# Performance work log

Hardware: AMD Instinct MI355X
Metric: run time of the kernel (lower is better)

Reference implementation:

```python
import jax, jax.numpy as jnp
import numpy as np

LATENT_DIM = 128
NUM_QUANTIZERS = 8
CODEBOOK_SIZE = 1024


def setup_inputs() -> dict:
    key = jax.random.key(0)
    k1, k2 = jax.random.split(key)
    z = jax.random.normal(k1, (8, LATENT_DIM, 4096), dtype=jnp.float32)
    scale = 1.0 / np.sqrt(LATENT_DIM)
    codebooks = jax.random.uniform(
        k2, (NUM_QUANTIZERS, CODEBOOK_SIZE, LATENT_DIM),
        minval=-scale, maxval=scale, dtype=jnp.float32)
    return {"z": z, "codebooks": codebooks}


def _nearest_indices(x_flat, codebook):
    # x_flat: [N, D], codebook: [K, D] -> [N] argmin of squared L2 distance
    d = (jnp.sum(x_flat * x_flat, axis=1, keepdims=True)
         - 2.0 * x_flat @ codebook.T
         + jnp.sum(codebook * codebook, axis=1)[None, :])
    return jnp.argmin(d, axis=1)


def reference(z, codebooks):
    # z: [B, D, S] -> z_bsd: [B, S, D]
    z_bsd = jnp.transpose(z, (0, 2, 1))
    B, S, D = z_bsd.shape
    Q, K, _ = codebooks.shape

    residual = z_bsd
    quantized = jnp.zeros_like(z_bsd)
    idx_list = []
    for q in range(Q):  # small fixed loop over quantizer stages
        cb = codebooks[q]
        idx = _nearest_indices(residual.reshape(-1, D), cb).reshape(B, S)
        selected = cb[idx]                       # [B, S, D] gather
        quantized = quantized + selected
        residual = residual - jax.lax.stop_gradient(selected)
        idx_list.append(idx)
    indices = jnp.stack(idx_list, axis=-1)        # [B, S, Q]

    commitment_loss = jnp.mean(
        (z_bsd - jax.lax.stop_gradient(quantized)) ** 2)
    quantized_st = z_bsd + jax.lax.stop_gradient(quantized - z_bsd)

    def _perplexity(ix):  # ix: [B, S] codes for one quantizer
        counts = jnp.zeros((K,), jnp.float32).at[ix.reshape(-1)].add(1.0)
        probs = counts / jnp.maximum(counts.sum(), 1.0)
        entropy = -jnp.sum(probs * jnp.log(probs + 1e-10))
        return jnp.exp(entropy)

    perplexity = jnp.mean(jax.vmap(_perplexity, in_axes=2)(indices))

    return (jnp.transpose(quantized_st, (0, 2, 1)),  # [B, D, S]
            indices, commitment_loss, perplexity)
```

## Files before the change

kernel.cpp:

```cpp
#include <hip/hip_runtime.h>
#include <math.h>
#include <stdint.h>

#define D       128
#define KCODES  1024
#define NQ      8
#define BATCH   8
#define SLEN    4096
#define NPTS    (BATCH*SLEN)
#define TM      64

typedef __attribute__((address_space(1))) const void GV;
typedef __attribute__((address_space(3))) void LV;
__device__ __forceinline__ void gload16(const void* g, void* l) {
    __builtin_amdgcn_global_load_lds((GV*)g, (LV*)l, 16, 0, 0);
}

__global__ void k_zero(int* hist, double* csum) {
    int t = blockIdx.x * blockDim.x + threadIdx.x;
    if (t < NQ * KCODES) hist[t] = 0;
    if (t == 0) *csum = 0.0;
}

__global__ void k_c2(const float* __restrict__ cbs, float* __restrict__ c2f) {
    int i = blockIdx.x * blockDim.x + threadIdx.x;
    const float* row = cbs + (size_t)i * D;
    float r8[8];
    #pragma unroll
    for (int j = 0; j < 8; ++j) r8[j] = __fmul_rn(row[j], row[j]);
    for (int d = 8; d < 128; d += 8)
        #pragma unroll
        for (int j = 0; j < 8; ++j)
            r8[j] = __fadd_rn(r8[j], __fmul_rn(row[d + j], row[d + j]));
    float s01 = __fadd_rn(r8[0], r8[1]);
    float s23 = __fadd_rn(r8[2], r8[3]);
    float s45 = __fadd_rn(r8[4], r8[5]);
    float s67 = __fadd_rn(r8[6], r8[7]);
    c2f[i] = __fadd_rn(__fadd_rn(s01, s23), __fadd_rn(s45, s67));
}

__global__ __launch_bounds__(256) void k_init(const float* __restrict__ z,
                                              float* __restrict__ resid,
                                              float* __restrict__ quant) {
    __shared__ float xt[64][129];
    int b = blockIdx.x >> 6, st = blockIdx.x & 63;
    int s0 = st * 64;
    for (int it = 0; it < 32; ++it) {
        int flat = it * 256 + threadIdx.x;
        int d = flat >> 6, sl = flat & 63;
        xt[sl][d] = z[((size_t)(b * D + d)) * SLEN + s0 + sl];
    }
    __syncthreads();
    for (int it = 0; it < 8; ++it) {
        int flat = it * 256 + threadIdx.x;
        int sl = flat >> 5, dq = (flat & 31) * 4;
        size_t o = (size_t)(b * SLEN + s0 + sl) * D + dq;
        float4 r;
        r.x = xt[sl][dq]; r.y = xt[sl][dq + 1];
        r.z = xt[sl][dq + 2]; r.w = xt[sl][dq + 3];
        *(float4*)(resid + o) = r;
        float4 zz; zz.x = zz.y = zz.z = zz.w = 0.0f;
        *(float4*)(quant + o) = zz;
    }
}

__global__ __launch_bounds__(256, 2) void k_argmin(const float* __restrict__ cb,
                                                   const float* __restrict__ c2,
                                                   const float* __restrict__ resid,
                                                   float* __restrict__ pbest,
                                                   int* __restrict__ pidx) {
    __shared__ __align__(16) float xs[TM][132];
    __shared__ __align__(16) float cs[4][2][512];
    __shared__ __align__(16) float ccl[4][128];
    __shared__ float redS[4][TM];
    __shared__ int   redI[4][TM];

    int tid = threadIdx.x;
    int u = blockIdx.x;
    int pblk = u >> 1, half = u & 1;
    int pbase = pblk * TM;
    int l = tid & 63, w = tid >> 6;
    int pl = l & 7, cl = l >> 3;

    const char* cwb = (const char*)cb + ((size_t)(half * 512 + w * 128) << 9);
    char* csw = (char*)&cs[w][0][0];
    const char* xsb = (const char*)&xs[0][0];

    int lanoff = ((l >> 1) << 9) + ((l & 1) << 4);

#define ISSUE(T) { \
    const char* _src = cwb + (((T) >> 4) << 15) + (((T) & 15) << 5) + lanoff; \
    char* _dst = csw + (((T) & 1) << 11); \
    gload16(_src,             _dst); \
    gload16(_src + (1 << 14), _dst + 1024); }

    ISSUE(0);
    if (l < 32) {
        float4 cv = *(const float4*)(c2 + half * 512 + w * 128 + l * 4);
        *(float4*)&ccl[w][l * 4] = cv;
    }

    #pragma unroll
    for (int it = 0; it < 8; ++it) {
        int e = (it * 256 + tid) * 4;
        int p = e >> 7, d = e & 127;
        *(float4*)&xs[p][d] = *(const float4*)(resid + (size_t)(pbase + p) * D + d);
    }
    __syncthreads();

    if (tid < TM) {
        float r8[8];
        #pragma unroll
        for (int j = 0; j < 8; ++j) r8[j] = __fmul_rn(xs[tid][j], xs[tid][j]);
        for (int i = 8; i < 128; i += 8)
            #pragma unroll
            for (int j = 0; j < 8; ++j)
                r8[j] = __fadd_rn(r8[j], __fmul_rn(xs[tid][i + j], xs[tid][i + j]));
        float s01 = __fadd_rn(r8[0], r8[1]);
        float s23 = __fadd_rn(r8[2], r8[3]);
        float s45 = __fadd_rn(r8[4], r8[5]);
        float s67 = __fadd_rn(r8[6], r8[7]);
        xs[tid][128] = __fadd_rn(__fadd_rn(s01, s23), __fadd_rn(s45, s67));
    }
    __syncthreads();

    float acc[8][8];
    #pragma unroll
    for (int i = 0; i < 8; ++i)
        #pragma unroll
        for (int j = 0; j < 8; ++j) acc[i][j] = 0.0f;
    float best[8]; int bidx[8];
    #pragma unroll
    for (int i = 0; i < 8; ++i) { best[i] = 3.4e38f; bidx[i] = 0; }

    #pragma unroll 1
    for (int t = 0; t < 32; ++t) {
        if (t < 31) {
            ISSUE(t + 1);
            asm volatile("s_waitcnt vmcnt(2)" ::: "memory");
        } else {
            asm volatile("s_waitcnt vmcnt(0)" ::: "memory");
        }
        const char* cbuf = csw + ((t & 1) << 11) + (cl << 5);
        const char* xrow = xsb + pl * 528 + ((t & 15) << 5);
        float4 cfa[8], cfb[8];
        #pragma unroll
        for (int j = 0; j < 8; ++j) {
            cfa[j] = *(const float4*)(cbuf + (j << 8));
            cfb[j] = *(const float4*)(cbuf + (j << 8) + 16);
        }
        #pragma unroll
        for (int i = 0; i < 8; ++i) {
            float4 xA = *(const float4*)(xrow + i * 4224);
            float4 xB = *(const float4*)(xrow + i * 4224 + 16);
            #pragma unroll
            for (int j = 0; j < 8; ++j) {
                float a = acc[i][j];
                a = __fmaf_rn(xA.x, cfa[j].x, a);
                a = __fmaf_rn(xA.y, cfa[j].y, a);
                a = __fmaf_rn(xA.z, cfa[j].z, a);
                a = __fmaf_rn(xA.w, cfa[j].w, a);
                a = __fmaf_rn(xB.x, cfb[j].x, a);
                a = __fmaf_rn(xB.y, cfb[j].y, a);
                a = __fmaf_rn(xB.z, cfb[j].z, a);
                a = __fmaf_rn(xB.w, cfb[j].w, a);
                acc[i][j] = a;
            }
        }
        if ((t & 15) == 15) {
            int c = t >> 4;
            #pragma unroll
            for (int i = 0; i < 8; ++i) {
                float xxv = xs[pl + 8 * i][128];
                #pragma unroll
                for (int j = 0; j < 8; ++j) {
                    float cc = ccl[w][(c << 6) + cl + (j << 3)];
                    int k = half * 512 + (w << 7) + (c << 6) + cl + (j << 3);
                    float t1  = __fadd_rn(xxv, __fmul_rn(-2.0f, acc[i][j]));
                    float dsc = __fadd_rn(t1, cc);
                    if (dsc < best[i]) { best[i] = dsc; bidx[i] = k; }
                    acc[i][j] = 0.0f;
                }
            }
        }
    }

    #pragma unroll
    for (int i = 0; i < 8; ++i) {
        float b = best[i]; int bi = bidx[i];
        #pragma unroll
        for (int off = 8; off < 64; off <<= 1) {
            float b2 = __shfl_xor(b, off, 64);
            int  bi2 = __shfl_xor(bi, off, 64);
            if (b2 < b || (b2 == b && bi2 < bi)) { b = b2; bi = bi2; }
        }
        if (cl == 0) { redS[w][pl + 8 * i] = b; redI[w][pl + 8 * i] = bi; }
    }
    __syncthreads();
    if (tid < TM) {
        float b = redS[0][tid]; int bi = redI[0][tid];
        #pragma unroll
        for (int ww = 1; ww < 4; ++ww) {
            float b2 = redS[ww][tid]; int bi2 = redI[ww][tid];
            if (b2 < b || (b2 == b && bi2 < bi)) { b = b2; bi = bi2; }
        }
        pbest[half * NPTS + pbase + tid] = b;
        pidx [half * NPTS + pbase + tid] = bi;
    }
#undef ISSUE
}

__global__ void k_update(const float* __restrict__ cb,
                         const float* __restrict__ pbest,
                         const int* __restrict__ pidx,
                         int* __restrict__ idx,
                         float* __restrict__ resid, float* __restrict__ quant) {
    int gid = blockIdx.x * blockDim.x + threadIdx.x;
    int n = gid >> 5, d4 = (gid & 31) * 4;
    float a = pbest[n], b = pbest[NPTS + n];
    int ia = pidx[n], ib = pidx[NPTS + n];
    int k = (b < a) ? ib : ia;
    if ((gid & 31) == 0) idx[n] = k;
    float4 c = *(const float4*)(cb + (size_t)k * D + d4);
    size_t o = (size_t)n * D + d4;
    float4 r = *(const float4*)(resid + o);
    float4 q = *(const float4*)(quant + o);
    r.x = __fsub_rn(r.x, c.x); r.y = __fsub_rn(r.y, c.y);
    r.z = __fsub_rn(r.z, c.z); r.w = __fsub_rn(r.w, c.w);
    q.x = __fadd_rn(q.x, c.x); q.y = __fadd_rn(q.y, c.y);
    q.z = __fadd_rn(q.z, c.z); q.w = __fadd_rn(q.w, c.w);
    *(float4*)(resid + o) = r;
    *(float4*)(quant + o) = q;
}

__global__ __launch_bounds__(256) void k_out0(const float* __restrict__ z,
                                              const float* __restrict__ quant,
                                              float* __restrict__ out0,
                                              double* __restrict__ csum) {
    __shared__ float xt[64][129];
    __shared__ double wsum[4];
    int b = blockIdx.x >> 6, st = blockIdx.x & 63;
    int s0 = st * 64;
    for (int it = 0; it < 8; ++it) {
        int flat = it * 256 + threadIdx.x;
        int sl = flat >> 5, dq = (flat & 31) * 4;
        float4 q = *(const float4*)(quant + (size_t)(b * SLEN + s0 + sl) * D + dq);
        xt[sl][dq] = q.x; xt[sl][dq + 1] = q.y;
        xt[sl][dq + 2] = q.z; xt[sl][dq + 3] = q.w;
    }
    __syncthreads();
    double v = 0.0;
    for (int it = 0; it < 32; ++it) {
        int flat = it * 256 + threadIdx.x;
        int d = flat >> 6, sl = flat & 63;
        size_t o = ((size_t)(b * D + d)) * SLEN + s0 + sl;
        float zz = z[o], qq = xt[sl][d];
        out0[o] = __fadd_rn(zz, __fsub_rn(qq, zz));
        float e = __fsub_rn(zz, qq);
        v += (double)e * (double)e;
    }
    for (int off = 32; off > 0; off >>= 1) v += __shfl_down(v, off, 64);
    int lane = threadIdx.x & 63, wv = threadIdx.x >> 6;
    if (lane == 0) wsum[wv] = v;
    __syncthreads();
    if (threadIdx.x == 0) {
        double tsum = wsum[0] + wsum[1] + wsum[2] + wsum[3];
        atomicAdd(csum, tsum);
    }
}

__global__ void k_outidx(const int* __restrict__ idx, float* __restrict__ out1) {
    int o = blockIdx.x * blockDim.x + threadIdx.x;
    int q = o & 7, n = o >> 3;
    out1[o] = (float)idx[q * NPTS + n];
}

__global__ void k_hist(const int* __restrict__ idx, int* __restrict__ hist) {
    int o = blockIdx.x * blockDim.x + threadIdx.x;
    int q = o >> 15;
    atomicAdd(&hist[q * KCODES + idx[o]], 1);
}

__global__ __launch_bounds__(256) void k_final(const int* __restrict__ hist,
                                               const double* __restrict__ csum,
                                               float* __restrict__ outs) {
    __shared__ double sh[256];
    double perp = 0.0;
    for (int q = 0; q < NQ; ++q) {
        double h = 0.0;
        for (int k = threadIdx.x; k < KCODES; k += 256) {
            double p = (double)hist[q * KCODES + k] / (double)NPTS;
            h -= p * log(p + 1e-10);
        }
        sh[threadIdx.x] = h; __syncthreads();
        for (int off = 128; off > 0; off >>= 1) {
            if (threadIdx.x < off) sh[threadIdx.x] += sh[threadIdx.x + off];
            __syncthreads();
        }
        if (threadIdx.x == 0) perp += exp(sh[0]);
        __syncthreads();
    }
    if (threadIdx.x == 0) {
        outs[0] = (float)(*csum / (double)((size_t)NPTS * D));
        outs[1] = (float)(perp / (double)NQ);
    }
}

extern "C" void kernel_launch(void* const* d_in, const int* in_sizes, int n_in,
                              void* d_out, int out_size, void* d_ws, size_t ws_size,
                              hipStream_t stream) {
    const float* z  = (const float*)d_in[0];
    const float* cb = (const float*)d_in[1];
    float* out0 = (float*)d_out;
    float* out1 = out0 + 4194304;
    float* outs = out1 + 262144;

    char* w = (char*)d_ws;
    float* resid  = (float*)w;
    float* quant  = (float*)(w + 16777216);
    int*   idx    = (int*)(w + 33554432);
    int*   hist   = (int*)(w + 34603008);
    double* csum  = (double*)(w + 34635776);
    float* c2f    = (float*)(w + 34635840);
    float* pbest  = (float*)(w + 34668608);
    int*   pidx   = (int*)(w + 34930752);

    k_zero<<<32, 256, 0, stream>>>(hist, csum);
    k_c2<<<32, 256, 0, stream>>>(cb, c2f);
    k_init<<<512, 256, 0, stream>>>(z, resid, quant);

    for (int q = 0; q < NQ; ++q) {
        const float* cbq = cb + (size_t)q * KCODES * D;
        k_argmin<<<2 * NPTS / TM, 256, 0, stream>>>(cbq, c2f + q * KCODES, resid,
                                                    pbest, pidx);
        k_update<<<NPTS * 32 / 256, 256, 0, stream>>>(cbq, pbest, pidx,
                                                      idx + q * NPTS, resid, quant);
    }

    k_out0<<<512, 256, 0, stream>>>(z, quant, out0, csum);
    k_outidx<<<NPTS * NQ / 256, 256, 0, stream>>>(idx, out1);
    k_hist<<<NPTS * NQ / 256, 256, 0, stream>>>(idx, hist);
    k_final<<<1, 256, 0, stream>>>(hist, csum, outs);
}
```

Measured before the change: 1.080 ms.

## Transpose residual tile in LDS and use packed FP32 FMA for distance dot products

```diff
diff --git a/kernel.cpp b/kernel.cpp
--- a/kernel.cpp
+++ b/kernel.cpp
@@ -10,11 +10,20 @@
 #define NPTS    (BATCH*SLEN)
 #define TM      64
 
+typedef __attribute__((ext_vector_type(2))) float f32x2;
+
 typedef __attribute__((address_space(1))) const void GV;
 typedef __attribute__((address_space(3))) void LV;
 __device__ __forceinline__ void gload16(const void* g, void* l) {
     __builtin_amdgcn_global_load_lds((GV*)g, (LV*)l, 16, 0, 0);
 }
+
+#define PKFMA_LO(A, X, CP) \
+    asm("v_pk_fma_f32 %0, %1, %2, %0 op_sel_hi:[1,0,1]" \
+        : "+v"(A) : "v"(X), "v"(CP))
+#define PKFMA_HI(A, X, CP) \
+    asm("v_pk_fma_f32 %0, %1, %2, %0 op_sel:[0,1,0] op_sel_hi:[1,1,1]" \
+        : "+v"(A) : "v"(X), "v"(CP))
 
 __global__ void k_zero(int* hist, double* csum) {
     int t = blockIdx.x * blockDim.x + threadIdx.x;
@@ -69,7 +78,7 @@
                                                    const float* __restrict__ resid,
                                                    float* __restrict__ pbest,
                                                    int* __restrict__ pidx) {
-    __shared__ __align__(16) float xs[TM][132];
+    __shared__ __align__(16) float xst[129][64];
     __shared__ __align__(16) float cs[4][2][512];
     __shared__ __align__(16) float ccl[4][128];
     __shared__ float redS[4][TM];
@@ -84,7 +93,7 @@
 
     const char* cwb = (const char*)cb + ((size_t)(half * 512 + w * 128) << 9);
     char* csw = (char*)&cs[w][0][0];
-    const char* xsb = (const char*)&xs[0][0];
+    float* xstf = &xst[0][0];
 
     int lanoff = ((l >> 1) << 9) + ((l & 1) << 4);
 
@@ -102,33 +111,41 @@
 
     #pragma unroll
     for (int it = 0; it < 8; ++it) {
-        int e = (it * 256 + tid) * 4;
-        int p = e >> 7, d = e & 127;
-        *(float4*)&xs[p][d] = *(const float4*)(resid + (size_t)(pbase + p) * D + d);
-    }
-    __syncthreads();
-
+        int g = it * 4 + w;
+        float4 v = *(const float4*)(resid + (size_t)(pbase + l) * D + 4 * g);
+        xstf[(size_t)(4 * g + 0) * 64 + l] = v.x;
+        xstf[(size_t)(4 * g + 1) * 64 + l] = v.y;
+        xstf[(size_t)(4 * g + 2) * 64 + l] = v.z;
+        xstf[(size_t)(4 * g + 3) * 64 + l] = v.w;
+    }
     if (tid < TM) {
+        const float* row = resid + (size_t)(pbase + tid) * D;
         float r8[8];
         #pragma unroll
-        for (int j = 0; j < 8; ++j) r8[j] = __fmul_rn(xs[tid][j], xs[tid][j]);
-        for (int i = 8; i < 128; i += 8)
-            #pragma unroll
-            for (int j = 0; j < 8; ++j)
-                r8[j] = __fadd_rn(r8[j], __fmul_rn(xs[tid][i + j], xs[tid][i + j]));
+        for (int j = 0; j < 8; ++j) r8[j] = 0.0f;
+        #pragma unroll
+        for (int g = 0; g < 32; ++g) {
+            float4 v = *(const float4*)(row + 4 * g);
+            int b = (g & 1) * 4;
+            r8[b + 0] = __fadd_rn(r8[b + 0], __fmul_rn(v.x, v.x));
+            r8[b + 1] = __fadd_rn(r8[b + 1], __fmul_rn(v.y, v.y));
+            r8[b + 2] = __fadd_rn(r8[b + 2], __fmul_rn(v.z, v.z));
+            r8[b + 3] = __fadd_rn(r8[b + 3], __fmul_rn(v.w, v.w));
+        }
         float s01 = __fadd_rn(r8[0], r8[1]);
         float s23 = __fadd_rn(r8[2], r8[3]);
         float s45 = __fadd_rn(r8[4], r8[5]);
         float s67 = __fadd_rn(r8[6], r8[7]);
-        xs[tid][128] = __fadd_rn(__fadd_rn(s01, s23), __fadd_rn(s45, s67));
-    }
-    __syncthreads();
-
-    float acc[8][8];
-    #pragma unroll
-    for (int i = 0; i < 8; ++i)
-        #pragma unroll
-        for (int j = 0; j < 8; ++j) acc[i][j] = 0.0f;
+        xstf[(size_t)128 * 64 + tid] = __fadd_rn(__fadd_rn(s01, s23),
+                                                 __fadd_rn(s45, s67));
+    }
+    __syncthreads();
+
+    f32x2 accp[4][8];
+    #pragma unroll
+    for (int m = 0; m < 4; ++m)
+        #pragma unroll
+        for (int j = 0; j < 8; ++j) { accp[m][j].x = 0.0f; accp[m][j].y = 0.0f; }
     float best[8]; int bidx[8];
     #pragma unroll
     for (int i = 0; i < 8; ++i) { best[i] = 3.4e38f; bidx[i] = 0; }
@@ -142,59 +159,80 @@
             asm volatile("s_waitcnt vmcnt(0)" ::: "memory");
         }
         const char* cbuf = csw + ((t & 1) << 11) + (cl << 5);
-        const char* xrow = xsb + pl * 528 + ((t & 15) << 5);
-        float4 cfa[8], cfb[8];
+        const float* xrow = xstf + (size_t)((t & 15) << 3) * 64 + (pl << 3);
+        f32x2 xA[8], xB[8], xC[8], xD[8];
+        #pragma unroll
+        for (int d = 0; d < 8; ++d) {
+            float4 q = *(const float4*)(xrow + (size_t)d * 64);
+            float4 r = *(const float4*)(xrow + (size_t)d * 64 + 4);
+            const f32x2* qp = (const f32x2*)&q;
+            const f32x2* rp = (const f32x2*)&r;
+            xA[d] = qp[0]; xB[d] = qp[1]; xC[d] = rp[0]; xD[d] = rp[1];
+        }
         #pragma unroll
         for (int j = 0; j < 8; ++j) {
-            cfa[j] = *(const float4*)(cbuf + (j << 8));
-            cfb[j] = *(const float4*)(cbuf + (j << 8) + 16);
-        }
-        #pragma unroll
-        for (int i = 0; i < 8; ++i) {
-            float4 xA = *(const float4*)(xrow + i * 4224);
-            float4 xB = *(const float4*)(xrow + i * 4224 + 16);
+            float4 cfa = *(const float4*)(cbuf + (j << 8));
+            float4 cfb = *(const float4*)(cbuf + (j << 8) + 16);
+            const f32x2* ca = (const f32x2*)&cfa;
+            const f32x2* cb2 = (const f32x2*)&cfb;
+            f32x2 a0 = accp[0][j], a1 = accp[1][j];
+            f32x2 a2 = accp[2][j], a3 = accp[3][j];
+            PKFMA_LO(a0, xA[0], ca[0]);  PKFMA_LO(a1, xB[0], ca[0]);
+            PKFMA_LO(a2, xC[0], ca[0]);  PKFMA_LO(a3, xD[0], ca[0]);
+            PKFMA_HI(a0, xA[1], ca[0]);  PKFMA_HI(a1, xB[1], ca[0]);
+            PKFMA_HI(a2, xC[1], ca[0]);  PKFMA_HI(a3, xD[1], ca[0]);
+            PKFMA_LO(a0, xA[2], ca[1]);  PKFMA_LO(a1, xB[2], ca[1]);
+            PKFMA_LO(a2, xC[2], ca[1]);  PKFMA_LO(a3, xD[2], ca[1]);
+            PKFMA_HI(a0, xA[3], ca[1]);  PKFMA_HI(a1, xB[3], ca[1]);
+            PKFMA_HI(a2, xC[3], ca[1]);  PKFMA_HI(a3, xD[3], ca[1]);
+            PKFMA_LO(a0, xA[4], cb2[0]); PKFMA_LO(a1, xB[4], cb2[0]);
+            PKFMA_LO(a2, xC[4], cb2[0]); PKFMA_LO(a3, xD[4], cb2[0]);
+            PKFMA_HI(a0, xA[5], cb2[0]); PKFMA_HI(a1, xB[5], cb2[0]);
+            PKFMA_HI(a2, xC[5], cb2[0]); PKFMA_HI(a3, xD[5], cb2[0]);
+            PKFMA_LO(a0, xA[6], cb2[1]); PKFMA_LO(a1, xB[6], cb2[1]);
+            PKFMA_LO(a2, xC[6], cb2[1]); PKFMA_LO(a3, xD[6], cb2[1]);
+            PKFMA_HI(a0, xA[7], cb2[1]); PKFMA_HI(a1, xB[7], cb2[1]);
+            PKFMA_HI(a2, xC[7], cb2[1]); PKFMA_HI(a3, xD[7], cb2[1]);
+            accp[0][j] = a0; accp[1][j] = a1;
+            accp[2][j] = a2; accp[3][j] = a3;
+        }
+        if ((t & 15) == 15) {
+            int c = t >> 4;
+            float xxv[8];
+            #pragma unroll
+            for (int lp = 0; lp < 8; ++lp)
+                xxv[lp] = xstf[(size_t)128 * 64 + 8 * pl + lp];
             #pragma unroll
             for (int j = 0; j < 8; ++j) {
-                float a = acc[i][j];
-                a = __fmaf_rn(xA.x, cfa[j].x, a);
-                a = __fmaf_rn(xA.y, cfa[j].y, a);
-                a = __fmaf_rn(xA.z, cfa[j].z, a);
-                a = __fmaf_rn(xA.w, cfa[j].w, a);
-                a = __fmaf_rn(xB.x, cfb[j].x, a);
-                a = __fmaf_rn(xB.y, cfb[j].y, a);
-                a = __fmaf_rn(xB.z, cfb[j].z, a);
-                a = __fmaf_rn(xB.w, cfb[j].w, a);
-                acc[i][j] = a;
-            }
-        }
-        if ((t & 15) == 15) {
-            int c = t >> 4;
-            #pragma unroll
-            for (int i = 0; i < 8; ++i) {
-                float xxv = xs[pl + 8 * i][128];
+                float cc = ccl[w][(c << 6) + cl + (j << 3)];
+                int k = half * 512 + (w << 7) + (c << 6) + cl + (j << 3);
                 #pragma unroll
-                for (int j = 0; j < 8; ++j) {
-                    float cc = ccl[w][(c << 6) + cl + (j << 3)];
-                    int k = half * 512 + (w << 7) + (c << 6) + cl + (j << 3);
-                    float t1  = __fadd_rn(xxv, __fmul_rn(-2.0f, acc[i][j]));
-                    float dsc = __fadd_rn(t1, cc);
-                    if (dsc < best[i]) { best[i] = dsc; bidx[i] = k; }
-                    acc[i][j] = 0.0f;
+                for (int m = 0; m < 4; ++m) {
+                    f32x2 av = accp[m][j];
+                    float t1, dsc;
+                    t1  = __fadd_rn(xxv[2 * m], __fmul_rn(-2.0f, av.x));
+                    dsc = __fadd_rn(t1, cc);
+                    if (dsc < best[2 * m])     { best[2 * m] = dsc;     bidx[2 * m] = k; }
+                    t1  = __fadd_rn(xxv[2 * m + 1], __fmul_rn(-2.0f, av.y));
+                    dsc = __fadd_rn(t1, cc);
+                    if (dsc < best[2 * m + 1]) { best[2 * m + 1] = dsc; bidx[2 * m + 1] = k; }
+                    av.x = 0.0f; av.y = 0.0f;
+                    accp[m][j] = av;
                 }
             }
         }
     }
 
     #pragma unroll
-    for (int i = 0; i < 8; ++i) {
-        float b = best[i]; int bi = bidx[i];
+    for (int lp = 0; lp < 8; ++lp) {
+        float b = best[lp]; int bi = bidx[lp];
         #pragma unroll
         for (int off = 8; off < 64; off <<= 1) {
             float b2 = __shfl_xor(b, off, 64);
             int  bi2 = __shfl_xor(bi, off, 64);
             if (b2 < b || (b2 == b && bi2 < bi)) { b = b2; bi = bi2; }
         }
-        if (cl == 0) { redS[w][pl + 8 * i] = b; redI[w][pl + 8 * i] = bi; }
+        if (cl == 0) { redS[w][8 * pl + lp] = b; redI[w][8 * pl + lp] = bi; }
     }
     __syncthreads();
     if (tid < TM) {
```

After: 1.018 ms. 1.06x faster.
